# Optimization experiments

Hardware: AMD Instinct MI355X
Metric: run time of the kernel (lower is better)

## Reference

```python
import jax, jax.numpy as jnp
import numpy as np


def setup_inputs() -> dict:
    key = jax.random.key(0)
    x = jax.random.normal(key, (16, 64, 256, 256), dtype=jnp.float32)
    return {"x": x}


def reference(x) -> jnp.ndarray:
    B, C, H, W = x.shape
    hw = H * W
    q = x.reshape(B, C, hw)          # proj_query: [B, C, HW]
    k = x.reshape(B, hw, C)          # proj_key: view (reshape), NOT transpose — faithful to source
    attn = jax.nn.softmax(jnp.einsum('bcn,bnd->bcd', q, k), axis=-1)  # [B, C, C]
    out = jnp.einsum('bcd,bdn->bcn', attn, q).reshape(B, C, H, W)
    return out + x
```

## Files before the change

### kernel.cpp

```cpp
#include <hip/hip_runtime.h>

#define B_   16
#define C_   64
#define HW_  65536
#define CHW_ (C_ * HW_)

typedef short bf16x8 __attribute__((ext_vector_type(8)));
typedef float f32x4v __attribute__((ext_vector_type(4)));

__device__ __forceinline__ unsigned short bfrne(float f) {
    unsigned int u = __float_as_uint(f);
    u += 0x7FFFu + ((u >> 16) & 1u);
    return (unsigned short)(u >> 16);
}
__device__ __forceinline__ float bfdec(unsigned short h) {
    return __uint_as_float((unsigned int)h << 16);
}

__global__ __launch_bounds__(256, 2) void k1_gram(const float* __restrict__ x,
                                                  float* __restrict__ partial,
                                                  int nch, int nb) {
    const int ch  = blockIdx.x;
    const int b   = blockIdx.y;
    const int t   = threadIdx.x;
    const int w   = t >> 6;
    const int l   = t & 63;
    const int g   = l >> 4;
    const int col = l & 15;

    const float* xb = x + (size_t)b * CHW_;
    const int nq  = nb >> 2;
    const int nw0 = ch * nb + w * nq;

    f32x4v acc[4][4];
    #pragma unroll
    for (int ct = 0; ct < 4; ct++)
        #pragma unroll
        for (int dt = 0; dt < 4; dt++) acc[ct][dt] = (f32x4v)(0.f);

    for (int ns = nw0; ns < nw0 + nq; ns += 32) {
        bf16x8 ahi[4], alo[4];
        #pragma unroll
        for (int ct = 0; ct < 4; ct++) {
            const float* ap = xb + (size_t)(16 * ct + col) * HW_ + ns + 8 * g;
            float av[8];
            *(float4*)&av[0] = *(const float4*)ap;
            *(float4*)&av[4] = *(const float4*)(ap + 4);
            #pragma unroll
            for (int j = 0; j < 8; j++) {
                const unsigned short h = bfrne(av[j]);
                ahi[ct][j] = (short)h;
                alo[ct][j] = (short)bfrne(av[j] - bfdec(h));
            }
        }
        bf16x8 bhi[4], blo[4];
        #pragma unroll
        for (int dt = 0; dt < 4; dt++) {
            const float* bp = xb + (size_t)(ns + 8 * g) * C_ + 16 * dt + col;
            float bv[8];
            #pragma unroll
            for (int j = 0; j < 8; j++) bv[j] = bp[j * C_];
            #pragma unroll
            for (int j = 0; j < 8; j++) {
                const unsigned short h = bfrne(bv[j]);
                bhi[dt][j] = (short)h;
                blo[dt][j] = (short)bfrne(bv[j] - bfdec(h));
            }
        }
        #pragma unroll
        for (int ct = 0; ct < 4; ct++)
            #pragma unroll
            for (int dt = 0; dt < 4; dt++) {
                acc[ct][dt] = __builtin_amdgcn_mfma_f32_16x16x32_bf16(
                    ahi[ct], bhi[dt], acc[ct][dt], 0, 0, 0);
                acc[ct][dt] = __builtin_amdgcn_mfma_f32_16x16x32_bf16(
                    ahi[ct], blo[dt], acc[ct][dt], 0, 0, 0);
                acc[ct][dt] = __builtin_amdgcn_mfma_f32_16x16x32_bf16(
                    alo[ct], bhi[dt], acc[ct][dt], 0, 0, 0);
            }
    }

    __shared__ float sred[4096];
    for (int wr = 0; wr < 4; wr++) {
        if (w == wr) {
            #pragma unroll
            for (int ct = 0; ct < 4; ct++)
                #pragma unroll
                for (int dt = 0; dt < 4; dt++)
                    #pragma unroll
                    for (int r = 0; r < 4; r++) {
                        const int idx = (16 * ct + 4 * g + r) * 64 + 16 * dt + col;
                        if (wr == 0) sred[idx] = acc[ct][dt][r];
                        else         sred[idx] += acc[ct][dt][r];
                    }
        }
        __syncthreads();
    }

    float* pb = partial + (size_t)(b * nch + ch) * 4096;
    for (int i = 4 * t; i < 4096; i += 1024)
        *(float4*)&pb[i] = *(const float4*)&sred[i];
}

__global__ __launch_bounds__(256) void k2_softmax(const float* __restrict__ partial,
                                                  unsigned short* __restrict__ mbf,
                                                  int nch) {
    const int c = blockIdx.x;
    const int b = blockIdx.y;
    const int t = threadIdx.x;
    const int w = t >> 6;
    const int d = t & 63;

    float s = 0.f;
    for (int ch = w; ch < nch; ch += 4)
        s += partial[(size_t)(b * nch + ch) * 4096 + c * 64 + d];

    __shared__ float red[256];
    red[t] = s;
    __syncthreads();
    if (w == 0) {
        s = red[d] + red[64 + d] + red[128 + d] + red[192 + d];
        float m = s;
        #pragma unroll
        for (int off = 32; off > 0; off >>= 1) m = fmaxf(m, __shfl_xor(m, off));
        const float e = expf(s - m);
        float sum = e;
        #pragma unroll
        for (int off = 32; off > 0; off >>= 1) sum += __shfl_xor(sum, off);
        mbf[(size_t)b * 4096 + c * 64 + d] = bfrne(e / sum + (c == d ? 1.f : 0.f));
    }
}

__global__ __launch_bounds__(256, 2) void k3_out(const float* __restrict__ x,
                                                 const unsigned short* __restrict__ mbf,
                                                 float* __restrict__ out) {
    const int nbk = blockIdx.x;
    const int b   = blockIdx.y;
    const int t   = threadIdx.x;
    const int w   = t >> 6;
    const int l   = t & 63;
    const int g   = l >> 4;
    const int col = l & 15;

    __shared__ float Xs[64 * 256];

    const int nblk = nbk * 256;
    const float* xb = x + (size_t)b * CHW_;

    #pragma unroll
    for (int i = 0; i < 16; i++) {
        const int d = 16 * w + i;
        const int p = ((d >> 3) & 1) << 2;
        const float* gp = xb + (size_t)d * HW_ + nblk + 4 * (l ^ p);
        __builtin_amdgcn_global_load_lds(
            (const __attribute__((address_space(1))) void*)gp,
            (__attribute__((address_space(3))) void*)(&Xs[d * 256]),
            16, 0, 0);
    }

    bf16x8 afr[4][2];
    const unsigned short* mb = mbf + (size_t)b * 4096;
    #pragma unroll
    for (int ct = 0; ct < 4; ct++)
        #pragma unroll
        for (int ks = 0; ks < 2; ks++)
            afr[ct][ks] = *(const bf16x8*)(mb + (16 * ct + col) * 64 + 32 * ks + 8 * g);

    __syncthreads();

    f32x4v acc[4][4];
    #pragma unroll
    for (int ct = 0; ct < 4; ct++)
        #pragma unroll
        for (int nt = 0; nt < 4; nt++)
            acc[ct][nt] = (f32x4v)(0.f);

    const int psw = (g & 1) << 2;

    #pragma unroll
    for (int nt = 0; nt < 4; nt++) {
        const int n  = 64 * w + 16 * nt + col;
        const int cn = n >> 2;
        const int eo = ((cn ^ psw) << 2) + (col & 3);

        bf16x8 bfr[2];
        #pragma unroll
        for (int ks = 0; ks < 2; ks++)
            #pragma unroll
            for (int j = 0; j < 8; j++) {
                const int r = 32 * ks + 8 * g + j;
                bfr[ks][j] = (short)bfrne(Xs[r * 256 + eo]);
            }

        #pragma unroll
        for (int ct = 0; ct < 4; ct++)
            #pragma unroll
            for (int ks = 0; ks < 2; ks++)
                acc[ct][nt] = __builtin_amdgcn_mfma_f32_16x16x32_bf16(
                    afr[ct][ks], bfr[ks], acc[ct][nt], 0, 0, 0);
    }

    float* ob = out + (size_t)b * CHW_;
    #pragma unroll
    for (int ct = 0; ct < 4; ct++)
        #pragma unroll
        for (int nt = 0; nt < 4; nt++)
            #pragma unroll
            for (int r = 0; r < 4; r++)
                ob[(size_t)(16 * ct + 4 * g + r) * HW_ + nblk + 64 * w + 16 * nt + col] =
                    acc[ct][nt][r];
}

extern "C" void kernel_launch(void* const* d_in, const int* in_sizes, int n_in,
                              void* d_out, int out_size, void* d_ws, size_t ws_size,
                              hipStream_t stream) {
    const float* x = (const float*)d_in[0];
    float* out = (float*)d_out;

    float* wsf          = (float*)d_ws;
    unsigned short* mbf = (unsigned short*)wsf;
    float* partial      = wsf + (size_t)B_ * 4096;

    int nch = 64;
    while (nch > 1) {
        size_t need = (size_t)B_ * 4096 * sizeof(float)
                    + (size_t)B_ * nch * 4096 * sizeof(float);
        if (need <= ws_size) break;
        nch >>= 1;
    }
    const int nb = HW_ / nch;

    k1_gram<<<dim3(nch, B_), 256, 0, stream>>>(x, partial, nch, nb);
    k2_softmax<<<dim3(C_, B_), 256, 0, stream>>>(partial, mbf, nch);
    k3_out<<<dim3(HW_ / 256, B_), 256, 0, stream>>>(x, mbf, out);
}
```

Before: 209.1 us.

## Double-buffer k1 key tiles in LDS via async global_load_lds prefetch

In the Gram kernel, the strided per-element global loads of the reshaped key operand are replaced by per-wave double-buffered async global-to-LDS copies of contiguous 32x64 tiles, with an XOR swizzle to avoid bank conflicts. The next tile is prefetched while the current one is converted and fed to MFMA, and manual s_waitcnt vmcnt waits sequence the loads. This targets uncoalesced memory access and load latency in k1. In exchange it uses more LDS per block, which the final reduction reuses, and it relies on a hand-counted vmcnt value being correct.

```diff
diff --git a/kernel.cpp b/kernel.cpp
--- a/kernel.cpp
+++ b/kernel.cpp
@@ -28,9 +28,27 @@
     const int g   = l >> 4;
     const int col = l & 15;
 
+    __shared__ float Bs[4][2][2048];
+
     const float* xb = x + (size_t)b * CHW_;
     const int nq  = nb >> 2;
     const int nw0 = ch * nb + w * nq;
+    const int nit = nq >> 5;
+
+#define K1_STAGE(dst, ns)                                                  \
+    {                                                                      \
+        const float* bsrc = xb + (size_t)(ns) * C_;                        \
+        _Pragma("unroll")                                                  \
+        for (int i = 0; i < 8; i++) {                                      \
+            const int sw = (i >> 1) << 2;                                  \
+            const float* gp = bsrc + 256 * i + 64 * (l >> 4)               \
+                              + 4 * ((l & 15) ^ sw);                       \
+            __builtin_amdgcn_global_load_lds(                              \
+                (const __attribute__((address_space(1))) void*)gp,         \
+                (__attribute__((address_space(3))) void*)((dst) + 256 * i),\
+                16, 0, 0);                                                 \
+        }                                                                  \
+    }
 
     f32x4v acc[4][4];
     #pragma unroll
@@ -38,49 +56,63 @@
         #pragma unroll
         for (int dt = 0; dt < 4; dt++) acc[ct][dt] = (f32x4v)(0.f);
 
-    for (int ns = nw0; ns < nw0 + nq; ns += 32) {
-        bf16x8 ahi[4], alo[4];
+    K1_STAGE(Bs[w][0], nw0);
+
+    for (int it = 0; it < nit; ++it) {
+        const int ns = nw0 + (it << 5);
+        float* cur = Bs[w][it & 1];
+        float* nxt = Bs[w][(it + 1) & 1];
+
+        float av[4][8];
         #pragma unroll
         for (int ct = 0; ct < 4; ct++) {
             const float* ap = xb + (size_t)(16 * ct + col) * HW_ + ns + 8 * g;
-            float av[8];
-            *(float4*)&av[0] = *(const float4*)ap;
-            *(float4*)&av[4] = *(const float4*)(ap + 4);
+            *(float4*)&av[ct][0] = *(const float4*)ap;
+            *(float4*)&av[ct][4] = *(const float4*)(ap + 4);
+        }
+
+        if (it + 1 < nit) K1_STAGE(nxt, ns + 32);
+
+        bf16x8 ahi[4], alo[4];
+        #pragma unroll
+        for (int ct = 0; ct < 4; ct++)
             #pragma unroll
             for (int j = 0; j < 8; j++) {
-                const unsigned short h = bfrne(av[j]);
+                const unsigned short h = bfrne(av[ct][j]);
                 ahi[ct][j] = (short)h;
-                alo[ct][j] = (short)bfrne(av[j] - bfdec(h));
-            }
-        }
-        bf16x8 bhi[4], blo[4];
+                alo[ct][j] = (short)bfrne(av[ct][j] - bfdec(h));
+            }
+
+        if (it + 1 < nit) asm volatile("s_waitcnt vmcnt(8)" ::: "memory");
+        else              asm volatile("s_waitcnt vmcnt(0)" ::: "memory");
+
         #pragma unroll
         for (int dt = 0; dt < 4; dt++) {
-            const float* bp = xb + (size_t)(ns + 8 * g) * C_ + 16 * dt + col;
+            const int eo = 16 * (dt ^ g) + col;
             float bv[8];
             #pragma unroll
-            for (int j = 0; j < 8; j++) bv[j] = bp[j * C_];
+            for (int j = 0; j < 8; j++) bv[j] = cur[(8 * g + j) * 64 + eo];
+            bf16x8 bhi, blo;
             #pragma unroll
             for (int j = 0; j < 8; j++) {
                 const unsigned short h = bfrne(bv[j]);
-                bhi[dt][j] = (short)h;
-                blo[dt][j] = (short)bfrne(bv[j] - bfdec(h));
+                bhi[j] = (short)h;
+                blo[j] = (short)bfrne(bv[j] - bfdec(h));
+            }
+            #pragma unroll
+            for (int ct = 0; ct < 4; ct++) {
+                acc[ct][dt] = __builtin_amdgcn_mfma_f32_16x16x32_bf16(
+                    ahi[ct], bhi, acc[ct][dt], 0, 0, 0);
+                acc[ct][dt] = __builtin_amdgcn_mfma_f32_16x16x32_bf16(
+                    ahi[ct], blo, acc[ct][dt], 0, 0, 0);
+                acc[ct][dt] = __builtin_amdgcn_mfma_f32_16x16x32_bf16(
+                    alo[ct], bhi, acc[ct][dt], 0, 0, 0);
             }
         }
-        #pragma unroll
-        for (int ct = 0; ct < 4; ct++)
-            #pragma unroll
-            for (int dt = 0; dt < 4; dt++) {
-                acc[ct][dt] = __builtin_amdgcn_mfma_f32_16x16x32_bf16(
-                    ahi[ct], bhi[dt], acc[ct][dt], 0, 0, 0);
-                acc[ct][dt] = __builtin_amdgcn_mfma_f32_16x16x32_bf16(
-                    ahi[ct], blo[dt], acc[ct][dt], 0, 0, 0);
-                acc[ct][dt] = __builtin_amdgcn_mfma_f32_16x16x32_bf16(
-                    alo[ct], bhi[dt], acc[ct][dt], 0, 0, 0);
-            }
-    }
-
-    __shared__ float sred[4096];
+    }
+#undef K1_STAGE
+
+    float* sred = (float*)Bs;
     for (int wr = 0; wr < 4; wr++) {
         if (w == wr) {
             #pragma unroll
```

Result: no change. 206.4 us (-1.3%).
